# Kernel optimization log

Measured on AMD Instinct MI355X. Metric: run time of the kernel, lower is better.

Reference implementation:

```python
import jax, jax.numpy as jnp
import numpy as np

B, T, D, H = 128, 1024, 128, 128

def setup_inputs() -> dict:
    key = jax.random.key(0)
    ks = jax.random.split(key, 7)
    scale = 0.05
    return {
        "x": jax.random.normal(ks[0], (B, T, D), dtype=jnp.float32),
        "h0": jnp.zeros((B, H), dtype=jnp.float32),
        "U": jax.random.normal(ks[1], (D, H), dtype=jnp.float32) * scale,
        "W": jax.random.normal(ks[2], (H, H), dtype=jnp.float32) * scale,
        "V": jax.random.normal(ks[3], (H, H), dtype=jnp.float32) * scale,
        "bu": jnp.zeros((H,), dtype=jnp.float32),
        "bw": jnp.zeros((H,), dtype=jnp.float32),
        "bv": jnp.zeros((H,), dtype=jnp.float32),
    }

def reference(x, h0, U, W, V, bu, bw, bv):
    # Precompute input projection for all timesteps in one big GEMM: [B,T,H]
    xu = jnp.einsum('btd,dh->bth', x, U) + bu

    def step(h, xu_t):
        # st = tanh(x@U + bu + h@W + bw)
        st = jnp.tanh(xu_t + h @ W + bw)
        # o = tanh(st@V + bv)
        o = jnp.tanh(st @ V + bv)
        return st, o

    # scan over time: xu transposed to [T,B,H]
    _, o_seq = jax.lax.scan(step, h0, jnp.swapaxes(xu, 0, 1))
    return jnp.swapaxes(o_seq, 0, 1)  # [B,T,H]
```

## Files before the change

### kernel.cpp

```cpp
#include <hip/hip_runtime.h>

#define B_ 128
#define T_ 1024
#define D_ 128
#define H_ 128

typedef short bf16x8 __attribute__((ext_vector_type(8)));
typedef float f32x4 __attribute__((ext_vector_type(4)));

__device__ inline unsigned cvt_pk_bf16(float lo, float hi) {
    unsigned r;
    asm("v_cvt_pk_bf16_f32 %0, %1, %2" : "=v"(r) : "v"(lo), "v"(hi));
    return r;
}

__device__ inline float fast_tanh(float x) {
    float e = __builtin_amdgcn_exp2f(x * 2.885390081777927f);
    float r = __builtin_amdgcn_rcpf(1.0f + e);
    return fmaf(-2.0f, r, 1.0f);
}

__device__ inline void lds_barrier() {
    asm volatile("s_waitcnt lgkmcnt(0)\n\ts_barrier" ::: "memory");
}

__global__ __launch_bounds__(256) void xu_kernel(
    const float* __restrict__ x, const float* __restrict__ U,
    const float* __restrict__ bu, const float* __restrict__ bw,
    float* __restrict__ out)
{
    __shared__ bf16x8 uf[2048];
    const int tid  = threadIdx.x;
    const int lane = tid & 63;
    const int wave = tid >> 6;
    const int q = lane >> 4, c = lane & 15;

    for (int s = tid; s < 2048; s += 256) {
        int l = s & 63, kk = (s >> 6) & 3, nt = s >> 8;
        int lq = l >> 4, lc = l & 15;
        int kbase = 32 * kk + 8 * lq;
        int col = 16 * nt + lc;
        float v[8];
#pragma unroll
        for (int j = 0; j < 8; ++j) v[j] = U[(kbase + j) * H_ + col];
        union { bf16x8 v8; unsigned u[4]; } f;
#pragma unroll
        for (int j = 0; j < 4; ++j) f.u[j] = cvt_pk_bf16(v[2 * j], v[2 * j + 1]);
        uf[s] = f.v8;
    }

    f32x4 bias4[8];
#pragma unroll
    for (int nt = 0; nt < 8; ++nt) {
        const int cb = 16 * nt + 4 * q;
        f32x4 a = *(const f32x4*)(bu + cb);
        f32x4 b = *(const f32x4*)(bw + cb);
#pragma unroll
        for (int r = 0; r < 4; ++r) bias4[nt][r] = a[r] + b[r];
    }

    __syncthreads();

    for (int it = 0; it < 4; ++it) {
        const int row0 = (blockIdx.x * 4 + it) * 64 + wave * 16;
        bf16x8 af[4];
#pragma unroll
        for (int kk = 0; kk < 4; ++kk) {
            const float* px = x + (size_t)(row0 + c) * D_ + 32 * kk + 8 * q;
            f32x4 a0 = *(const f32x4*)px;
            f32x4 a1 = *(const f32x4*)(px + 4);
            union { bf16x8 v8; unsigned u[4]; } f;
            f.u[0] = cvt_pk_bf16(a0[0], a0[1]);
            f.u[1] = cvt_pk_bf16(a0[2], a0[3]);
            f.u[2] = cvt_pk_bf16(a1[0], a1[1]);
            f.u[3] = cvt_pk_bf16(a1[2], a1[3]);
            af[kk] = f.v8;
        }
        float* po = out + (size_t)(row0 + c) * H_ + 4 * q;
#pragma unroll
        for (int nt = 0; nt < 8; ++nt) {
            f32x4 acc = bias4[nt];
#pragma unroll
            for (int kk = 0; kk < 4; ++kk)
                acc = __builtin_amdgcn_mfma_f32_16x16x32_bf16(
                    uf[(nt * 4 + kk) * 64 + lane], af[kk], acc, 0, 0, 0);
            *(f32x4*)(po + 16 * nt) = acc;
        }
    }
}

__global__ __launch_bounds__(256) void scan_kernel(
    const float* __restrict__ xu_in, float* __restrict__ st_out,
    const float* __restrict__ h0, const float* __restrict__ W)
{
    __shared__ __align__(16) short st[2][16][136];

    const int tid  = threadIdx.x;
    const int lane = tid & 63;
    const int wave = tid >> 6;
    const int q = lane >> 4, c = lane & 15;
    const int b0 = blockIdx.x * 16;
    const int cw = wave * 32 + 4 * q;

    bf16x8 wf[2][4];
#pragma unroll
    for (int tt = 0; tt < 2; ++tt) {
        const int c0 = wave * 32 + tt * 16;
#pragma unroll
        for (int kk = 0; kk < 4; ++kk) {
            const int kbase = 32 * kk + 8 * q;
            float v[8];
#pragma unroll
            for (int j = 0; j < 8; ++j) v[j] = W[(kbase + j) * H_ + c0 + c];
            union { bf16x8 v8; unsigned u[4]; } f;
#pragma unroll
            for (int j = 0; j < 4; ++j) f.u[j] = cvt_pk_bf16(v[2 * j], v[2 * j + 1]);
            wf[tt][kk] = f.v8;
        }
    }

    {
        const int m = tid >> 4, k0 = (tid & 15) * 8;
        const float* ph = h0 + (size_t)(b0 + m) * H_ + k0;
        f32x4 a0 = *(const f32x4*)ph;
        f32x4 a1 = *(const f32x4*)(ph + 4);
        union { bf16x8 v8; unsigned u[4]; } f;
        f.u[0] = cvt_pk_bf16(a0[0], a0[1]);
        f.u[1] = cvt_pk_bf16(a0[2], a0[3]);
        f.u[2] = cvt_pk_bf16(a1[0], a1[1]);
        f.u[3] = cvt_pk_bf16(a1[2], a1[3]);
        *(bf16x8*)&st[1][m][k0] = f.v8;
    }

    const float* xup = xu_in + ((size_t)(b0 + c) * T_) * H_ + cw;
    f32x4 xub[8][2];
    {
        const float* pp = xup;
#pragma unroll
        for (int u = 0; u < 8; ++u) {
            xub[u][0] = *(const f32x4*)pp;
            xub[u][1] = *(const f32x4*)(pp + 16);
            pp += H_;
        }
    }
    const float* pf = xup + 8 * H_;

    uint2 pkg0, pkg1;
    char* pst = (char*)st_out + (((size_t)(b0 + c) * T_) * H_) * 4 + cw * 2;

    const f32x4 z4 = {0.f, 0.f, 0.f, 0.f};

    lds_barrier();

    for (int tb = 0; tb < T_ / 8; ++tb) {
#pragma unroll
        for (int u = 0; u < 8; ++u) {
            const int t = tb * 8 + u;
            const int pr = (u + 1) & 1;
            const int pw = u & 1;

            if (t > 0) {
                *(uint2*)pst = pkg0;
                *(uint2*)(pst + 32) = pkg1;
                pst += H_ * 4;
            }

            f32x4 xu0 = xub[u][0], xu1 = xub[u][1];
            if (t < T_ - 8) {
                xub[u][0] = *(const f32x4*)pf;
                xub[u][1] = *(const f32x4*)(pf + 16);
                pf += H_;
            }

            bf16x8 af[4];
#pragma unroll
            for (int kk = 0; kk < 4; ++kk)
                af[kk] = *(const bf16x8*)&st[pr][c][32 * kk + 8 * q];

            f32x4 aA = __builtin_amdgcn_mfma_f32_16x16x32_bf16(wf[0][0], af[0], xu0, 0, 0, 0);
            f32x4 aB = __builtin_amdgcn_mfma_f32_16x16x32_bf16(wf[0][1], af[1], z4,  0, 0, 0);
            f32x4 bA = __builtin_amdgcn_mfma_f32_16x16x32_bf16(wf[1][0], af[0], xu1, 0, 0, 0);
            f32x4 bB = __builtin_amdgcn_mfma_f32_16x16x32_bf16(wf[1][1], af[1], z4,  0, 0, 0);
            aA = __builtin_amdgcn_mfma_f32_16x16x32_bf16(wf[0][2], af[2], aA, 0, 0, 0);
            aB = __builtin_amdgcn_mfma_f32_16x16x32_bf16(wf[0][3], af[3], aB, 0, 0, 0);
            bA = __builtin_amdgcn_mfma_f32_16x16x32_bf16(wf[1][2], af[2], bA, 0, 0, 0);
            bB = __builtin_amdgcn_mfma_f32_16x16x32_bf16(wf[1][3], af[3], bB, 0, 0, 0);

            float s0 = fast_tanh(aA[0] + aB[0]);
            float s1 = fast_tanh(aA[1] + aB[1]);
            float s2 = fast_tanh(aA[2] + aB[2]);
            float s3 = fast_tanh(aA[3] + aB[3]);
            float s4 = fast_tanh(bA[0] + bB[0]);
            float s5 = fast_tanh(bA[1] + bB[1]);
            float s6 = fast_tanh(bA[2] + bB[2]);
            float s7 = fast_tanh(bA[3] + bB[3]);

            pkg0.x = cvt_pk_bf16(s0, s1);
            pkg0.y = cvt_pk_bf16(s2, s3);
            pkg1.x = cvt_pk_bf16(s4, s5);
            pkg1.y = cvt_pk_bf16(s6, s7);

            *(uint2*)&st[pw][c][cw]      = pkg0;
            *(uint2*)&st[pw][c][cw + 16] = pkg1;

            lds_barrier();
        }
    }
    *(uint2*)pst = pkg0;
    *(uint2*)(pst + 32) = pkg1;
}

__global__ __launch_bounds__(256) void o_kernel(
    const float* __restrict__ st_in, float* __restrict__ o_out,
    const float* __restrict__ V, const float* __restrict__ bv)
{
    __shared__ bf16x8 vf[2048];
    const int tid  = threadIdx.x;
    const int lane = tid & 63;
    const int wave = tid >> 6;
    const int q = lane >> 4, c = lane & 15;

    for (int s = tid; s < 2048; s += 256) {
        int l = s & 63, kk = (s >> 6) & 3, nt = s >> 8;
        int lq = l >> 4, lc = l & 15;
        int kbase = 32 * kk + 8 * lq;
        int col = 16 * nt + lc;
        float v[8];
#pragma unroll
        for (int j = 0; j < 8; ++j) v[j] = V[(kbase + j) * H_ + col];
        union { bf16x8 v8; unsigned u[4]; } f;
#pragma unroll
        for (int j = 0; j < 4; ++j) f.u[j] = cvt_pk_bf16(v[2 * j], v[2 * j + 1]);
        vf[s] = f.v8;
    }

    f32x4 bias4[8];
#pragma unroll
    for (int nt = 0; nt < 8; ++nt)
        bias4[nt] = *(const f32x4*)(bv + 16 * nt + 4 * q);

    __syncthreads();

    for (int it = 0; it < 4; ++it) {
        const int row0 = (blockIdx.x * 4 + it) * 64 + wave * 16;
        const char* pa = (const char*)st_in + (size_t)(row0 + c) * (H_ * 4);
        bf16x8 af[4];
#pragma unroll
        for (int kk = 0; kk < 4; ++kk)
            af[kk] = *(const bf16x8*)(pa + 64 * kk + 16 * q);
        float* po = o_out + (size_t)(row0 + c) * H_ + 4 * q;
#pragma unroll
        for (int nt = 0; nt < 8; ++nt) {
            f32x4 acc = bias4[nt];
#pragma unroll
            for (int kk = 0; kk < 4; ++kk)
                acc = __builtin_amdgcn_mfma_f32_16x16x32_bf16(
                    vf[(nt * 4 + kk) * 64 + lane], af[kk], acc, 0, 0, 0);
            f32x4 o;
#pragma unroll
            for (int r = 0; r < 4; ++r) o[r] = fast_tanh(acc[r]);
            *(f32x4*)(po + 16 * nt) = o;
        }
    }
}

extern "C" void kernel_launch(void* const* d_in, const int* in_sizes, int n_in,
                              void* d_out, int out_size, void* d_ws, size_t ws_size,
                              hipStream_t stream) {
    const float* x  = (const float*)d_in[0];
    const float* h0 = (const float*)d_in[1];
    const float* U  = (const float*)d_in[2];
    const float* W  = (const float*)d_in[3];
    const float* V  = (const float*)d_in[4];
    const float* bu = (const float*)d_in[5];
    const float* bw = (const float*)d_in[6];
    const float* bv = (const float*)d_in[7];
    float* out = (float*)d_out;

    xu_kernel<<<512, 256, 0, stream>>>(x, U, bu, bw, out);
    scan_kernel<<<8, 256, 0, stream>>>(out, out, h0, W);
    o_kernel<<<512, 256, 0, stream>>>(out, out, V, bv);
}
```

Baseline: 802.5 us.

## Interleave two batch groups per scan block to hide recurrence latency

The scan kernel now handles 32 batch rows per block as two independent 16-row groups. Each time step issues both groups' MFMA chains and tanh work between the same LDS barriers, so each barrier covers twice the work. Only 4 blocks are launched instead of 8, and the xu prefetch depth drops from 8 steps to 4. The aim is to overlap the latency of the two independent recurrences, at the cost of using half as many CUs and doing more work per step on the serial critical path.

```diff
diff --git a/kernel.cpp b/kernel.cpp
--- a/kernel.cpp
+++ b/kernel.cpp
@@ -89,17 +89,17 @@
     }
 }
 
-__global__ __launch_bounds__(256) void scan_kernel(
+__global__ __launch_bounds__(256, 1) void scan_kernel(
     const float* __restrict__ xu_in, float* __restrict__ st_out,
     const float* __restrict__ h0, const float* __restrict__ W)
 {
-    __shared__ __align__(16) short st[2][16][136];
+    __shared__ __align__(16) short st[2][2][16][136];
 
     const int tid  = threadIdx.x;
     const int lane = tid & 63;
     const int wave = tid >> 6;
     const int q = lane >> 4, c = lane & 15;
-    const int b0 = blockIdx.x * 16;
+    const int b0 = blockIdx.x * 32;
     const int cw = wave * 32 + 4 * q;
 
     bf16x8 wf[2][4];
@@ -121,32 +121,36 @@
 
     {
         const int m = tid >> 4, k0 = (tid & 15) * 8;
-        const float* ph = h0 + (size_t)(b0 + m) * H_ + k0;
-        f32x4 a0 = *(const f32x4*)ph;
-        f32x4 a1 = *(const f32x4*)(ph + 4);
-        union { bf16x8 v8; unsigned u[4]; } f;
-        f.u[0] = cvt_pk_bf16(a0[0], a0[1]);
-        f.u[1] = cvt_pk_bf16(a0[2], a0[3]);
-        f.u[2] = cvt_pk_bf16(a1[0], a1[1]);
-        f.u[3] = cvt_pk_bf16(a1[2], a1[3]);
-        *(bf16x8*)&st[1][m][k0] = f.v8;
-    }
-
-    const float* xup = xu_in + ((size_t)(b0 + c) * T_) * H_ + cw;
-    f32x4 xub[8][2];
-    {
-        const float* pp = xup;
-#pragma unroll
-        for (int u = 0; u < 8; ++u) {
-            xub[u][0] = *(const f32x4*)pp;
-            xub[u][1] = *(const f32x4*)(pp + 16);
-            pp += H_;
-        }
-    }
-    const float* pf = xup + 8 * H_;
-
-    uint2 pkg0, pkg1;
-    char* pst = (char*)st_out + (((size_t)(b0 + c) * T_) * H_) * 4 + cw * 2;
+#pragma unroll
+        for (int g = 0; g < 2; ++g) {
+            const float* ph = h0 + (size_t)(b0 + 16 * g + m) * H_ + k0;
+            f32x4 a0 = *(const f32x4*)ph;
+            f32x4 a1 = *(const f32x4*)(ph + 4);
+            union { bf16x8 v8; unsigned u[4]; } f;
+            f.u[0] = cvt_pk_bf16(a0[0], a0[1]);
+            f.u[1] = cvt_pk_bf16(a0[2], a0[3]);
+            f.u[2] = cvt_pk_bf16(a1[0], a1[1]);
+            f.u[3] = cvt_pk_bf16(a1[2], a1[3]);
+            *(bf16x8*)&st[g][1][m][k0] = f.v8;
+        }
+    }
+
+    f32x4 xub[2][4][2];
+    const char* pfb[2];
+    char* psb[2];
+#pragma unroll
+    for (int g = 0; g < 2; ++g) {
+        const float* xup = xu_in + ((size_t)(b0 + 16 * g + c) * T_) * H_ + cw;
+#pragma unroll
+        for (int u = 0; u < 4; ++u) {
+            xub[g][u][0] = *(const f32x4*)(xup + u * H_);
+            xub[g][u][1] = *(const f32x4*)(xup + u * H_ + 16);
+        }
+        pfb[g] = (const char*)(xup + 4 * H_);
+        psb[g] = (char*)st_out + ((size_t)(b0 + 16 * g + c) * T_) * H_ * 4 + cw * 2;
+    }
+
+    uint2 pkg[2][2][2];
 
     const f32x4 z4 = {0.f, 0.f, 0.f, 0.f};
 
@@ -158,56 +162,78 @@
             const int t = tb * 8 + u;
             const int pr = (u + 1) & 1;
             const int pw = u & 1;
+            const int pb = (u + 1) & 1;
+            const int pc = u & 1;
+
+            bf16x8 af[2][4];
+#pragma unroll
+            for (int g = 0; g < 2; ++g)
+#pragma unroll
+                for (int kk = 0; kk < 4; ++kk)
+                    af[g][kk] = *(const bf16x8*)&st[g][pr][c][32 * kk + 8 * q];
 
             if (t > 0) {
-                *(uint2*)pst = pkg0;
-                *(uint2*)(pst + 32) = pkg1;
-                pst += H_ * 4;
+#pragma unroll
+                for (int g = 0; g < 2; ++g) {
+                    *(uint2*)(psb[g] + (u - 1) * 512)      = pkg[g][0][pb];
+                    *(uint2*)(psb[g] + (u - 1) * 512 + 32) = pkg[g][1][pb];
+                }
             }
 
-            f32x4 xu0 = xub[u][0], xu1 = xub[u][1];
-            if (t < T_ - 8) {
-                xub[u][0] = *(const f32x4*)pf;
-                xub[u][1] = *(const f32x4*)(pf + 16);
-                pf += H_;
+            f32x4 xuc[2][2];
+#pragma unroll
+            for (int g = 0; g < 2; ++g) {
+                xuc[g][0] = xub[g][u & 3][0];
+                xuc[g][1] = xub[g][u & 3][1];
             }
-
-            bf16x8 af[4];
-#pragma unroll
-            for (int kk = 0; kk < 4; ++kk)
-                af[kk] = *(const bf16x8*)&st[pr][c][32 * kk + 8 * q];
-
-            f32x4 aA = __builtin_amdgcn_mfma_f32_16x16x32_bf16(wf[0][0], af[0], xu0, 0, 0, 0);
-            f32x4 aB = __builtin_amdgcn_mfma_f32_16x16x32_bf16(wf[0][1], af[1], z4,  0, 0, 0);
-            f32x4 bA = __builtin_amdgcn_mfma_f32_16x16x32_bf16(wf[1][0], af[0], xu1, 0, 0, 0);
-            f32x4 bB = __builtin_amdgcn_mfma_f32_16x16x32_bf16(wf[1][1], af[1], z4,  0, 0, 0);
-            aA = __builtin_amdgcn_mfma_f32_16x16x32_bf16(wf[0][2], af[2], aA, 0, 0, 0);
-            aB = __builtin_amdgcn_mfma_f32_16x16x32_bf16(wf[0][3], af[3], aB, 0, 0, 0);
-            bA = __builtin_amdgcn_mfma_f32_16x16x32_bf16(wf[1][2], af[2], bA, 0, 0, 0);
-            bB = __builtin_amdgcn_mfma_f32_16x16x32_bf16(wf[1][3], af[3], bB, 0, 0, 0);
-
-            float s0 = fast_tanh(aA[0] + aB[0]);
-            float s1 = fast_tanh(aA[1] + aB[1]);
-            float s2 = fast_tanh(aA[2] + aB[2]);
-            float s3 = fast_tanh(aA[3] + aB[3]);
-            float s4 = fast_tanh(bA[0] + bB[0]);
-            float s5 = fast_tanh(bA[1] + bB[1]);
-            float s6 = fast_tanh(bA[2] + bB[2]);
-            float s7 = fast_tanh(bA[3] + bB[3]);
-
-            pkg0.x = cvt_pk_bf16(s0, s1);
-            pkg0.y = cvt_pk_bf16(s2, s3);
-            pkg1.x = cvt_pk_bf16(s4, s5);
-            pkg1.y = cvt_pk_bf16(s6, s7);
-
-            *(uint2*)&st[pw][c][cw]      = pkg0;
-            *(uint2*)&st[pw][c][cw + 16] = pkg1;
+            if (t + 4 < T_) {
+#pragma unroll
+                for (int g = 0; g < 2; ++g) {
+                    xub[g][u & 3][0] = *(const f32x4*)(pfb[g] + u * 512);
+                    xub[g][u & 3][1] = *(const f32x4*)(pfb[g] + u * 512 + 64);
+                }
+            }
+
+#pragma unroll
+            for (int g = 0; g < 2; ++g) {
+                f32x4 aA = __builtin_amdgcn_mfma_f32_16x16x32_bf16(wf[0][0], af[g][0], xuc[g][0], 0, 0, 0);
+                f32x4 aB = __builtin_amdgcn_mfma_f32_16x16x32_bf16(wf[0][1], af[g][1], z4,       0, 0, 0);
+                f32x4 bA = __builtin_amdgcn_mfma_f32_16x16x32_bf16(wf[1][0], af[g][0], xuc[g][1], 0, 0, 0);
+                f32x4 bB = __builtin_amdgcn_mfma_f32_16x16x32_bf16(wf[1][1], af[g][1], z4,       0, 0, 0);
+                aA = __builtin_amdgcn_mfma_f32_16x16x32_bf16(wf[0][2], af[g][2], aA, 0, 0, 0);
+                aB = __builtin_amdgcn_mfma_f32_16x16x32_bf16(wf[0][3], af[g][3], aB, 0, 0, 0);
+                bA = __builtin_amdgcn_mfma_f32_16x16x32_bf16(wf[1][2], af[g][2], bA, 0, 0, 0);
+                bB = __builtin_amdgcn_mfma_f32_16x16x32_bf16(wf[1][3], af[g][3], bB, 0, 0, 0);
+
+                float s0 = fast_tanh(aA[0] + aB[0]);
+                float s1 = fast_tanh(aA[1] + aB[1]);
+                float s2 = fast_tanh(aA[2] + aB[2]);
+                float s3 = fast_tanh(aA[3] + aB[3]);
+                float s4 = fast_tanh(bA[0] + bB[0]);
+                float s5 = fast_tanh(bA[1] + bB[1]);
+                float s6 = fast_tanh(bA[2] + bB[2]);
+                float s7 = fast_tanh(bA[3] + bB[3]);
+
+                pkg[g][0][pc].x = cvt_pk_bf16(s0, s1);
+                pkg[g][0][pc].y = cvt_pk_bf16(s2, s3);
+                pkg[g][1][pc].x = cvt_pk_bf16(s4, s5);
+                pkg[g][1][pc].y = cvt_pk_bf16(s6, s7);
+
+                *(uint2*)&st[g][pw][c][cw]      = pkg[g][0][pc];
+                *(uint2*)&st[g][pw][c][cw + 16] = pkg[g][1][pc];
+            }
 
             lds_barrier();
         }
-    }
-    *(uint2*)pst = pkg0;
-    *(uint2*)(pst + 32) = pkg1;
+#pragma unroll
+        for (int g = 0; g < 2; ++g) { pfb[g] += 4096; psb[g] += 4096; }
+    }
+
+#pragma unroll
+    for (int g = 0; g < 2; ++g) {
+        *(uint2*)(psb[g] - 512)      = pkg[g][0][1];
+        *(uint2*)(psb[g] - 512 + 32) = pkg[g][1][1];
+    }
 }
 
 __global__ __launch_bounds__(256) void o_kernel(
@@ -278,6 +304,6 @@
     float* out = (float*)d_out;
 
     xu_kernel<<<512, 256, 0, stream>>>(x, U, bu, bw, out);
-    scan_kernel<<<8, 256, 0, stream>>>(out, out, h0, W);
+    scan_kernel<<<4, 256, 0, stream>>>(out, out, h0, W);
     o_kernel<<<512, 256, 0, stream>>>(out, out, V, bv);
 }
```

New measurement: 1.253 ms. +56.1%, slower.

## Run scan with single wave per batch tile, keeping hidden state in registers

Applied to the files above, without the earlier changes.

The recurrent scan now uses one 64-lane wave per 16-row batch tile instead of four waves. The full W matrix is held as MFMA fragments in registers, and W's columns are permuted so each step's MFMA output lands directly in the next step's operand layout. This removes the per-timestep LDS round trip and block barrier from the serial critical path. In exchange one wave now issues all 32 MFMAs and 32 tanh per step, which lengthens the per-step dependency chain and reduces latency hiding.

```diff
diff --git a/kernel.cpp b/kernel.cpp
--- a/kernel.cpp
+++ b/kernel.cpp
@@ -18,10 +18,6 @@
     float e = __builtin_amdgcn_exp2f(x * 2.885390081777927f);
     float r = __builtin_amdgcn_rcpf(1.0f + e);
     return fmaf(-2.0f, r, 1.0f);
-}
-
-__device__ inline void lds_barrier() {
-    asm volatile("s_waitcnt lgkmcnt(0)\n\ts_barrier" ::: "memory");
 }
 
 __global__ __launch_bounds__(256) void xu_kernel(
@@ -89,39 +85,80 @@
     }
 }
 
-__global__ __launch_bounds__(256) void scan_kernel(
+__device__ __forceinline__ void scan_step(
+    const bf16x8 (&wf)[8][4],
+    const bf16x8 (&afIn)[4], bf16x8 (&afOut)[4],
+    const f32x4 (&cur)[8], f32x4 (&nxt)[8],
+    bool pref, const float*& prow, char*& pst, int q)
+{
+    if (pref) {
+#pragma unroll
+        for (int ntp = 0; ntp < 4; ++ntp) {
+            nxt[2 * ntp]     = *(const f32x4*)(prow + 32 * ntp + 8 * q);
+            nxt[2 * ntp + 1] = *(const f32x4*)(prow + 32 * ntp + 8 * q + 4);
+        }
+        prow += H_;
+    }
+
+#pragma unroll
+    for (int ntp = 0; ntp < 4; ++ntp) {
+        f32x4 a0 = cur[2 * ntp];
+        f32x4 a1 = cur[2 * ntp + 1];
+#pragma unroll
+        for (int kk = 0; kk < 4; ++kk) {
+            a0 = __builtin_amdgcn_mfma_f32_16x16x32_bf16(wf[2 * ntp][kk],     afIn[kk], a0, 0, 0, 0);
+            a1 = __builtin_amdgcn_mfma_f32_16x16x32_bf16(wf[2 * ntp + 1][kk], afIn[kk], a1, 0, 0, 0);
+        }
+        float s0 = fast_tanh(a0[0]);
+        float s1 = fast_tanh(a0[1]);
+        float s2 = fast_tanh(a0[2]);
+        float s3 = fast_tanh(a0[3]);
+        float s4 = fast_tanh(a1[0]);
+        float s5 = fast_tanh(a1[1]);
+        float s6 = fast_tanh(a1[2]);
+        float s7 = fast_tanh(a1[3]);
+
+        union { bf16x8 v8; unsigned u[4]; } f;
+        f.u[0] = cvt_pk_bf16(s0, s1);
+        f.u[1] = cvt_pk_bf16(s2, s3);
+        f.u[2] = cvt_pk_bf16(s4, s5);
+        f.u[3] = cvt_pk_bf16(s6, s7);
+        afOut[ntp] = f.v8;
+
+        *(bf16x8*)(pst + 64 * ntp + 16 * q) = f.v8;
+    }
+    pst += H_ * 4;
+}
+
+__global__ __launch_bounds__(64, 1) void scan_kernel(
     const float* __restrict__ xu_in, float* __restrict__ st_out,
     const float* __restrict__ h0, const float* __restrict__ W)
 {
-    __shared__ __align__(16) short st[2][16][136];
-
-    const int tid  = threadIdx.x;
-    const int lane = tid & 63;
-    const int wave = tid >> 6;
+    const int lane = threadIdx.x;
     const int q = lane >> 4, c = lane & 15;
     const int b0 = blockIdx.x * 16;
-    const int cw = wave * 32 + 4 * q;
-
-    bf16x8 wf[2][4];
-#pragma unroll
-    for (int tt = 0; tt < 2; ++tt) {
-        const int c0 = wave * 32 + tt * 16;
+
+    bf16x8 wf[8][4];
+#pragma unroll
+    for (int nt = 0; nt < 8; ++nt) {
+        const int wcol = 32 * (nt >> 1) + 4 * (nt & 1) + 8 * (c >> 2) + (c & 3);
 #pragma unroll
         for (int kk = 0; kk < 4; ++kk) {
             const int kbase = 32 * kk + 8 * q;
             float v[8];
 #pragma unroll
-            for (int j = 0; j < 8; ++j) v[j] = W[(kbase + j) * H_ + c0 + c];
+            for (int j = 0; j < 8; ++j) v[j] = W[(kbase + j) * H_ + wcol];
             union { bf16x8 v8; unsigned u[4]; } f;
 #pragma unroll
             for (int j = 0; j < 4; ++j) f.u[j] = cvt_pk_bf16(v[2 * j], v[2 * j + 1]);
-            wf[tt][kk] = f.v8;
-        }
-    }
-
-    {
-        const int m = tid >> 4, k0 = (tid & 15) * 8;
-        const float* ph = h0 + (size_t)(b0 + m) * H_ + k0;
+            wf[nt][kk] = f.v8;
+        }
+    }
+
+    bf16x8 afA[4], afB[4];
+#pragma unroll
+    for (int kk = 0; kk < 4; ++kk) {
+        const float* ph = h0 + (size_t)(b0 + c) * H_ + 32 * kk + 8 * q;
         f32x4 a0 = *(const f32x4*)ph;
         f32x4 a1 = *(const f32x4*)(ph + 4);
         union { bf16x8 v8; unsigned u[4]; } f;
@@ -129,85 +166,24 @@
         f.u[1] = cvt_pk_bf16(a0[2], a0[3]);
         f.u[2] = cvt_pk_bf16(a1[0], a1[1]);
         f.u[3] = cvt_pk_bf16(a1[2], a1[3]);
-        *(bf16x8*)&st[1][m][k0] = f.v8;
-    }
-
-    const float* xup = xu_in + ((size_t)(b0 + c) * T_) * H_ + cw;
-    f32x4 xub[8][2];
-    {
-        const float* pp = xup;
-#pragma unroll
-        for (int u = 0; u < 8; ++u) {
-            xub[u][0] = *(const f32x4*)pp;
-            xub[u][1] = *(const f32x4*)(pp + 16);
-            pp += H_;
-        }
-    }
-    const float* pf = xup + 8 * H_;
-
-    uint2 pkg0, pkg1;
-    char* pst = (char*)st_out + (((size_t)(b0 + c) * T_) * H_) * 4 + cw * 2;
-
-    const f32x4 z4 = {0.f, 0.f, 0.f, 0.f};
-
-    lds_barrier();
-
-    for (int tb = 0; tb < T_ / 8; ++tb) {
-#pragma unroll
-        for (int u = 0; u < 8; ++u) {
-            const int t = tb * 8 + u;
-            const int pr = (u + 1) & 1;
-            const int pw = u & 1;
-
-            if (t > 0) {
-                *(uint2*)pst = pkg0;
-                *(uint2*)(pst + 32) = pkg1;
-                pst += H_ * 4;
-            }
-
-            f32x4 xu0 = xub[u][0], xu1 = xub[u][1];
-            if (t < T_ - 8) {
-                xub[u][0] = *(const f32x4*)pf;
-                xub[u][1] = *(const f32x4*)(pf + 16);
-                pf += H_;
-            }
-
-            bf16x8 af[4];
-#pragma unroll
-            for (int kk = 0; kk < 4; ++kk)
-                af[kk] = *(const bf16x8*)&st[pr][c][32 * kk + 8 * q];
-
-            f32x4 aA = __builtin_amdgcn_mfma_f32_16x16x32_bf16(wf[0][0], af[0], xu0, 0, 0, 0);
-            f32x4 aB = __builtin_amdgcn_mfma_f32_16x16x32_bf16(wf[0][1], af[1], z4,  0, 0, 0);
-            f32x4 bA = __builtin_amdgcn_mfma_f32_16x16x32_bf16(wf[1][0], af[0], xu1, 0, 0, 0);
-            f32x4 bB = __builtin_amdgcn_mfma_f32_16x16x32_bf16(wf[1][1], af[1], z4,  0, 0, 0);
-            aA = __builtin_amdgcn_mfma_f32_16x16x32_bf16(wf[0][2], af[2], aA, 0, 0, 0);
-            aB = __builtin_amdgcn_mfma_f32_16x16x32_bf16(wf[0][3], af[3], aB, 0, 0, 0);
-            bA = __builtin_amdgcn_mfma_f32_16x16x32_bf16(wf[1][2], af[2], bA, 0, 0, 0);
-            bB = __builtin_amdgcn_mfma_f32_16x16x32_bf16(wf[1][3], af[3], bB, 0, 0, 0);
-
-            float s0 = fast_tanh(aA[0] + aB[0]);
-            float s1 = fast_tanh(aA[1] + aB[1]);
-            float s2 = fast_tanh(aA[2] + aB[2]);
-            float s3 = fast_tanh(aA[3] + aB[3]);
-            float s4 = fast_tanh(bA[0] + bB[0]);
-            float s5 = fast_tanh(bA[1] + bB[1]);
-            float s6 = fast_tanh(bA[2] + bB[2]);
-            float s7 = fast_tanh(bA[3] + bB[3]);
-
-            pkg0.x = cvt_pk_bf16(s0, s1);
-            pkg0.y = cvt_pk_bf16(s2, s3);
-            pkg1.x = cvt_pk_bf16(s4, s5);
-            pkg1.y = cvt_pk_bf16(s6, s7);
-
-            *(uint2*)&st[pw][c][cw]      = pkg0;
-            *(uint2*)&st[pw][c][cw + 16] = pkg1;
-
-            lds_barrier();
-        }
-    }
-    *(uint2*)pst = pkg0;
-    *(uint2*)(pst + 32) = pkg1;
+        afA[kk] = f.v8;
+    }
+
+    const float* prow = xu_in + (size_t)(b0 + c) * T_ * H_;
+    f32x4 curA[8], curB[8];
+#pragma unroll
+    for (int ntp = 0; ntp < 4; ++ntp) {
+        curA[2 * ntp]     = *(const f32x4*)(prow + 32 * ntp + 8 * q);
+        curA[2 * ntp + 1] = *(const f32x4*)(prow + 32 * ntp + 8 * q + 4);
+    }
+    prow += H_;
+
+    char* pst = (char*)st_out + (size_t)(b0 + c) * T_ * H_ * 4;
+
+    for (int t = 0; t < T_; t += 2) {
+        scan_step(wf, afA, afB, curA, curB, true,       prow, pst, q);
+        scan_step(wf, afB, afA, curB, curA, t + 2 < T_, prow, pst, q);
+    }
 }
 
 __global__ __launch_bounds__(256) void o_kernel(
@@ -278,6 +254,6 @@
     float* out = (float*)d_out;
 
     xu_kernel<<<512, 256, 0, stream>>>(x, U, bu, bw, out);
-    scan_kernel<<<8, 256, 0, stream>>>(out, out, h0, W);
+    scan_kernel<<<8, 64, 0, stream>>>(out, out, h0, W);
     o_kernel<<<512, 256, 0, stream>>>(out, out, V, bv);
 }
```

Result: slower. 1.102 ms (+37.3%).
